# Kernel optimization log

Measured on AMD Instinct MI355X. Metric: run time of the kernel, lower is better.

## Reference

```python
import jax, jax.numpy as jnp
import numpy as np

M_SIGMA = 1.0 * 0.997 / 3.0  # args.m * 0.997 / 3


def setup_inputs() -> dict:
    key = jax.random.key(0)
    k1, k2 = jax.random.split(key)
    B, D = 64, 512        # batch (sketches+shapes), embedding dim
    P = 256               # points per cloud
    embeddings = jax.random.normal(k1, (B, D), dtype=jnp.float32)
    xyz = jax.random.normal(k2, (B, P, 3), dtype=jnp.float32)
    return {"embeddings": embeddings, "xyz": xyz}


def _chamfer_all_pairs(shapes):
    # shapes: [M, P, 3]. Returns cd[i, j] = chamfer(shapes[i], shapes[j]),
    # chamfer = mean_p min_q ||x_p - y_q||^2 + mean_q min_p ||x_p - y_q||^2
    sq = jnp.sum(shapes * shapes, axis=-1)                  # [M, P]
    inner = jnp.einsum('ipd,jqd->ijpq', shapes, shapes)     # [M, M, P, P]
    d2 = sq[:, None, :, None] + sq[None, :, None, :] - 2.0 * inner
    cd = jnp.min(d2, axis=3).mean(axis=2) + jnp.min(d2, axis=2).mean(axis=2)
    return cd  # [M, M]


def reference(embeddings, xyz):
    # L2-normalize embeddings along feature dim
    emb = embeddings / jnp.linalg.norm(embeddings, axis=1, keepdims=True)
    B = emb.shape[0]
    mb = B // 2
    shapes = xyz[mb:]                                       # [mb, P, 3]
    sketch_feat, shape_feat = emb[:mb], emb[mb:]            # [mb, D] each
    inner_dot = sketch_feat @ shape_feat.T                  # [mb, mb]
    cd = _chamfer_all_pairs(shapes)                         # [mb, mb]
    real_dist = (cd ** 2) / (2.0 * M_SIGMA ** 2)
    p = jax.nn.softmax(-real_dist, axis=1)
    p_hat = jax.nn.softmax(inner_dot, axis=1)               # use_softmax=True
    reg = jnp.mean(jnp.abs(p_hat - p))                      # use_KL=False
    return reg
```

## Files before the change

kernel.cpp:

```cpp
#include <hip/hip_runtime.h>
#include <math.h>


__device__ __forceinline__ float waveReduceSum64(float v) {
    #pragma unroll
    for (int m = 32; m > 0; m >>= 1) v += __shfl_xor(v, m, 64);
    return v;
}

__global__ __launch_bounds__(256) void pairs_kernel(const float* __restrict__ emb,
                                                    const float* __restrict__ xyz,
                                                    float* __restrict__ cd,
                                                    float* __restrict__ dots) {
    const int t = threadIdx.x;
    const int b = blockIdx.x;

    __shared__ float4 SA[256];
    __shared__ float4 SB[256];
    __shared__ float  red[16];

    if (b < 528) {
        int i = 0, rem = b;
        while (rem >= (32 - i)) { rem -= (32 - i); ++i; }
        const int j = i + rem;

        const float* Pi = xyz + (32 + i) * 768;
        const float* Pj = xyz + (32 + j) * 768;

        SA[t] = make_float4(Pi[3*t], Pi[3*t+1], Pi[3*t+2], 0.0f);
        SB[t] = make_float4(Pj[3*t], Pj[3*t+1], Pj[3*t+2], 0.0f);
        __syncthreads();

        const float4 P = SA[t];
        const float4 Q = SB[t];
        float minA = 3.4e38f;
        float minB = 3.4e38f;
        #pragma unroll 8
        for (int s = 0; s < 256; ++s) {
            const float4 a  = SA[s];
            const float4 bb = SB[s];
            float dx = P.x - bb.x, dy = P.y - bb.y, dz = P.z - bb.z;
            float dA = dx*dx + dy*dy + dz*dz;
            float ex = Q.x - a.x,  ey = Q.y - a.y,  ez = Q.z - a.z;
            float dB = ex*ex + ey*ey + ez*ez;
            minA = fminf(minA, dA);
            minB = fminf(minB, dB);
        }

        float v = waveReduceSum64(minA + minB);
        if ((t & 63) == 0) red[t >> 6] = v;
        __syncthreads();
        if (t == 0) {
            float s = (red[0] + red[1] + red[2] + red[3]) * (1.0f / 256.0f);
            cd[i * 32 + j] = s;
            cd[j * 32 + i] = s;
        }
    } else {
        const int i = b - 528;
        float* rowi = (float*)SA;
        const float* Ei = emb + i * 512;
        rowi[t]       = Ei[t];
        rowi[t + 256] = Ei[t + 256];
        __syncthreads();

        const int w    = t >> 6;
        const int lane = t & 63;

        float ni = 0.0f;
        #pragma unroll
        for (int m = 0; m < 8; ++m) { float a = rowi[lane + 64*m]; ni += a*a; }
        ni = waveReduceSum64(ni);

        for (int j = w; j < 32; j += 4) {
            const float* Ej = emb + (32 + j) * 512;
            float dot = 0.0f, nj = 0.0f;
            #pragma unroll
            for (int m = 0; m < 8; ++m) {
                float a  = rowi[lane + 64*m];
                float bv = Ej[lane + 64*m];
                dot += a * bv;
                nj  += bv * bv;
            }
            dot = waveReduceSum64(dot);
            nj  = waveReduceSum64(nj);
            if (lane == 0) dots[i * 32 + j] = dot * rsqrtf(ni * nj);
        }
    }
}

__global__ __launch_bounds__(1024) void finish_kernel(const float* __restrict__ cd,
                                                      const float* __restrict__ dots,
                                                      float* __restrict__ out) {
    const int t = threadIdx.x;
    const float inv_denom = 1.0f / (2.0f * (0.997f / 3.0f) * (0.997f / 3.0f));

    float c = cd[t];
    float s = -(c * c) * inv_denom;
    float h = dots[t];

    float m1 = s;
    #pragma unroll
    for (int k = 16; k > 0; k >>= 1) m1 = fmaxf(m1, __shfl_xor(m1, k, 32));
    float e1 = expf(s - m1);
    float sum1 = e1;
    #pragma unroll
    for (int k = 16; k > 0; k >>= 1) sum1 += __shfl_xor(sum1, k, 32);
    float p = e1 / sum1;

    float m2 = h;
    #pragma unroll
    for (int k = 16; k > 0; k >>= 1) m2 = fmaxf(m2, __shfl_xor(m2, k, 32));
    float e2 = expf(h - m2);
    float sum2 = e2;
    #pragma unroll
    for (int k = 16; k > 0; k >>= 1) sum2 += __shfl_xor(sum2, k, 32);
    float ph = e2 / sum2;

    float a = fabsf(ph - p);
    a = waveReduceSum64(a);

    __shared__ float red[16];
    if ((t & 63) == 0) red[t >> 6] = a;
    __syncthreads();
    if (t == 0) {
        float tot = 0.0f;
        #pragma unroll
        for (int k = 0; k < 16; ++k) tot += red[k];
        out[0] = tot * (1.0f / 1024.0f);
    }
}

extern "C" void kernel_launch(void* const* d_in, const int* in_sizes, int n_in,
                              void* d_out, int out_size, void* d_ws, size_t ws_size,
                              hipStream_t stream) {
    const float* emb = (const float*)d_in[0];
    const float* xyz = (const float*)d_in[1];
    float* cd   = (float*)d_ws;
    float* dots = cd + 1024;
    float* out  = (float*)d_out;

    hipLaunchKernelGGL(pairs_kernel, dim3(560), dim3(256), 0, stream, emb, xyz, cd, dots);
    hipLaunchKernelGGL(finish_kernel, dim3(1), dim3(1024), 0, stream, cd, dots, out);
}
```

Baseline: 82.71 us.

## Split chamfer pairs into per-direction blocks with SoA LDS and packed math

Each off-diagonal chamfer pair is now computed by two blocks, one per nearest-neighbour direction, and the diagonal pairs are skipped because their distance is zero. The finish kernel sums the two halves. Shared memory moves from float4 AoS to separate x/y/z arrays read four points at a time. Distances use 2-wide float vectors so the compiler can emit packed FP32 math. The aim is more blocks to fill the CUs, less LDS traffic and less duplicated work, at the cost of an extra global combine and index arithmetic in the finish kernel.

```diff
diff --git a/kernel.cpp b/kernel.cpp
--- a/kernel.cpp
+++ b/kernel.cpp
@@ -1,6 +1,8 @@
 #include <hip/hip_runtime.h>
 #include <math.h>
 
+
+typedef float f32x2 __attribute__((ext_vector_type(2)));
 
 __device__ __forceinline__ float waveReduceSum64(float v) {
     #pragma unroll
@@ -10,54 +12,66 @@
 
 __global__ __launch_bounds__(256) void pairs_kernel(const float* __restrict__ emb,
                                                     const float* __restrict__ xyz,
-                                                    float* __restrict__ cd,
+                                                    float* __restrict__ cdHalf,
                                                     float* __restrict__ dots) {
     const int t = threadIdx.x;
     const int b = blockIdx.x;
 
-    __shared__ float4 SA[256];
-    __shared__ float4 SB[256];
-    __shared__ float  red[16];
+    __shared__ __align__(16) float S[3 * 256];
+    __shared__ float red[4];
+    float* Sx = S;
+    float* Sy = S + 256;
+    float* Sz = S + 512;
 
-    if (b < 528) {
-        int i = 0, rem = b;
-        while (rem >= (32 - i)) { rem -= (32 - i); ++i; }
-        const int j = i + rem;
+    if (b < 992) {
+        const int pb  = b >> 1;
+        const int dir = b & 1;
+        int i = 0, rem = pb;
+        while (rem >= (31 - i)) { rem -= (31 - i); ++i; }
+        const int j = i + 1 + rem;
 
-        const float* Pi = xyz + (32 + i) * 768;
-        const float* Pj = xyz + (32 + j) * 768;
+        const int outer = dir ? j : i;
+        const int inner = dir ? i : j;
 
-        SA[t] = make_float4(Pi[3*t], Pi[3*t+1], Pi[3*t+2], 0.0f);
-        SB[t] = make_float4(Pj[3*t], Pj[3*t+1], Pj[3*t+2], 0.0f);
+        const float* Po = xyz + (32 + outer) * 768;
+        const float* Pi = xyz + (32 + inner) * 768;
+
+        const float ix = Pi[3*t], iy = Pi[3*t+1], iz = Pi[3*t+2];
+        Sx[t] = ix; Sy[t] = iy; Sz[t] = iz;
+        const float px = Po[3*t], py = Po[3*t+1], pz = Po[3*t+2];
         __syncthreads();
 
-        const float4 P = SA[t];
-        const float4 Q = SB[t];
-        float minA = 3.4e38f;
-        float minB = 3.4e38f;
-        #pragma unroll 8
-        for (int s = 0; s < 256; ++s) {
-            const float4 a  = SA[s];
-            const float4 bb = SB[s];
-            float dx = P.x - bb.x, dy = P.y - bb.y, dz = P.z - bb.z;
-            float dA = dx*dx + dy*dy + dz*dz;
-            float ex = Q.x - a.x,  ey = Q.y - a.y,  ez = Q.z - a.z;
-            float dB = ex*ex + ey*ey + ez*ez;
-            minA = fminf(minA, dA);
-            minB = fminf(minB, dB);
+        const f32x2 Px = {px, px}, Py = {py, py}, Pz = {pz, pz};
+        f32x2 m0 = {3.4e38f, 3.4e38f}, m1 = {3.4e38f, 3.4e38f};
+
+        #pragma unroll 4
+        for (int s = 0; s < 256; s += 4) {
+            const float4 vx = *(const float4*)&Sx[s];
+            const float4 vy = *(const float4*)&Sy[s];
+            const float4 vz = *(const float4*)&Sz[s];
+            {
+                const f32x2 bx = {vx.x, vx.y}, by = {vy.x, vy.y}, bz = {vz.x, vz.y};
+                f32x2 dx = Px - bx, dy = Py - by, dz = Pz - bz;
+                f32x2 d = dx*dx + dy*dy + dz*dz;
+                m0.x = fminf(m0.x, d.x); m0.y = fminf(m0.y, d.y);
+            }
+            {
+                const f32x2 bx = {vx.z, vx.w}, by = {vy.z, vy.w}, bz = {vz.z, vz.w};
+                f32x2 dx = Px - bx, dy = Py - by, dz = Pz - bz;
+                f32x2 d = dx*dx + dy*dy + dz*dz;
+                m1.x = fminf(m1.x, d.x); m1.y = fminf(m1.y, d.y);
+            }
         }
+        const float mn = fminf(fminf(m0.x, m0.y), fminf(m1.x, m1.y));
 
-        float v = waveReduceSum64(minA + minB);
+        float v = waveReduceSum64(mn);
         if ((t & 63) == 0) red[t >> 6] = v;
         __syncthreads();
-        if (t == 0) {
-            float s = (red[0] + red[1] + red[2] + red[3]) * (1.0f / 256.0f);
-            cd[i * 32 + j] = s;
-            cd[j * 32 + i] = s;
-        }
+        if (t == 0)
+            cdHalf[b] = (red[0] + red[1] + red[2] + red[3]) * (1.0f / 256.0f);
     } else {
-        const int i = b - 528;
-        float* rowi = (float*)SA;
+        const int i = b - 992;
+        float* rowi = S;
         const float* Ei = emb + i * 512;
         rowi[t]       = Ei[t];
         rowi[t + 256] = Ei[t + 256];
@@ -88,13 +102,22 @@
     }
 }
 
-__global__ __launch_bounds__(1024) void finish_kernel(const float* __restrict__ cd,
+__global__ __launch_bounds__(1024) void finish_kernel(const float* __restrict__ cdHalf,
                                                       const float* __restrict__ dots,
                                                       float* __restrict__ out) {
     const int t = threadIdx.x;
+    const int i = t >> 5;
+    const int j = t & 31;
     const float inv_denom = 1.0f / (2.0f * (0.997f / 3.0f) * (0.997f / 3.0f));
 
-    float c = cd[t];
+    float c;
+    if (i == j) {
+        c = 0.0f;
+    } else {
+        const int a  = min(i, j), bb = max(i, j);
+        const int pb = a * 31 - (a * (a - 1)) / 2 + (bb - a - 1);
+        c = cdHalf[2 * pb] + cdHalf[2 * pb + 1];
+    }
     float s = -(c * c) * inv_denom;
     float h = dots[t];
 
@@ -135,10 +158,10 @@
                               hipStream_t stream) {
     const float* emb = (const float*)d_in[0];
     const float* xyz = (const float*)d_in[1];
-    float* cd   = (float*)d_ws;
-    float* dots = cd + 1024;
-    float* out  = (float*)d_out;
+    float* cdHalf = (float*)d_ws;
+    float* dots   = cdHalf + 1024;
+    float* out    = (float*)d_out;
 
-    hipLaunchKernelGGL(pairs_kernel, dim3(560), dim3(256), 0, stream, emb, xyz, cd, dots);
-    hipLaunchKernelGGL(finish_kernel, dim3(1), dim3(1024), 0, stream, cd, dots, out);
+    hipLaunchKernelGGL(pairs_kernel, dim3(1024), dim3(256), 0, stream, emb, xyz, cdHalf, dots);
+    hipLaunchKernelGGL(finish_kernel, dim3(1), dim3(1024), 0, stream, cdHalf, dots, out);
 }
```

New measurement: 66.22 us. 1.25x faster.
